# Performance work log

Measured on AMD Instinct MI355X. Metric: run time of the kernel, lower is better.

The kernel has to match this reference:

```python
import jax, jax.numpy as jnp
import numpy as np

B = 4096          # events
L = 524288        # total set points (avg 128 per event)
CIN = 16          # per-point feature size (set feature 'a')
DVEC = 32         # flat feature size (feature 'b')
PHI = [128, 128, 64]
MLP = [256, 128]
EPS = 1e-5        # BatchNorm1d eps


def setup_inputs() -> dict:
    key = jax.random.key(0)
    ks = jax.random.split(key, 10)
    def n(k, shape, scale=0.05):
        return jax.random.normal(k, shape, dtype=jnp.float32) * scale
    return {
        "x_a": jax.random.normal(ks[0], (1, CIN, L), dtype=jnp.float32),
        "x_b": jax.random.normal(ks[1], (B, DVEC), dtype=jnp.float32),
        # row 0 -> counts for set feature 'a'; row 1 ignored (Reshape branch)
        "sample_indices": jnp.full((2, B), L // B, dtype=jnp.int32),
        "W1": n(ks[2], (PHI[0], CIN)),  "b1": jnp.zeros((PHI[0],), jnp.float32),
        "W2": n(ks[3], (PHI[1], PHI[0])), "b2": jnp.zeros((PHI[1],), jnp.float32),
        "W3": n(ks[4], (PHI[2], PHI[1])), "b3": jnp.zeros((PHI[2],), jnp.float32),
        "Wm1": n(ks[5], (MLP[0], PHI[2] + DVEC)), "bm1": jnp.zeros((MLP[0],), jnp.float32),
        "g1": jnp.ones((MLP[0],), jnp.float32), "be1": jnp.zeros((MLP[0],), jnp.float32),
        "Wm2": n(ks[6], (MLP[1], MLP[0])), "bm2": jnp.zeros((MLP[1],), jnp.float32),
        "g2": jnp.ones((MLP[1],), jnp.float32), "be2": jnp.zeros((MLP[1],), jnp.float32),
        "Wm3": n(ks[7], (1, MLP[1])), "bm3": jnp.zeros((1,), jnp.float32),
    }


def _bn(x, g, b):
    # BatchNorm1d, training-mode batch stats, biased variance (torch semantics)
    mu = jnp.mean(x, axis=0)
    var = jnp.var(x, axis=0)
    return (x - mu) * jax.lax.rsqrt(var + EPS) * g + b


def reference(x_a, x_b, sample_indices,
              W1, b1, W2, b2, W3, b3,
              Wm1, bm1, g1, be1, Wm2, bm2, g2, be2, Wm3, bm3):
    counts = sample_indices[0].astype(jnp.int32)                       # [B]
    bounds = jnp.concatenate([jnp.zeros((1,), jnp.int32), jnp.cumsum(counts)])  # [B+1]

    # PhiNet: pointwise Conv1d stack (kernel size 1) on [CIN, L]
    h = x_a[0]
    h = jax.nn.relu(jnp.einsum('oc,cl->ol', W1, h) + b1[:, None])
    h = jax.nn.relu(jnp.einsum('oc,cl->ol', W2, h) + b2[:, None])
    h = jax.nn.relu(jnp.einsum('oc,cl->ol', W3, h) + b3[:, None])      # [64, L]

    # fused segment-mean: point p belongs to segment j iff bounds[j] <= p < bounds[j+1]
    seg = jnp.searchsorted(bounds, jnp.arange(h.shape[1], dtype=jnp.int32), side='right') - 1
    sums = jax.ops.segment_sum(h.T, seg, num_segments=counts.shape[0])  # [B, 64]
    means = sums / jnp.maximum(counts, 1).astype(jnp.float32)[:, None]

    # feature order: sorted keys -> ('a' set repr, 'b' flat)
    z = jnp.concatenate([means, x_b.reshape(-1, DVEC)], axis=1)        # [B, 96]

    z = jax.nn.relu(_bn(z @ Wm1.T + bm1, g1, be1))
    z = jax.nn.relu(_bn(z @ Wm2.T + bm2, g2, be2))
    return jax.nn.sigmoid(z @ Wm3.T + bm3)                             # [B, 1]
```

## Files before the change

kernel.cpp:

```cpp
#include <hip/hip_runtime.h>
#include <hip/hip_bf16.h>

#define B_EVENTS 4096
#define L_PTS    524288
#define CIN      16
#define C1       128
#define C2       128
#define C3       64
#define DVEC     32
#define ZDIM     96
#define M1       256
#define M2       128
#define BN_EPS   1e-5f
#define TPTS     64

typedef __attribute__((ext_vector_type(8))) short bf16x8;
typedef __attribute__((ext_vector_type(4))) float f32x4;

__device__ __forceinline__ ushort f2bf(float x) {
    union { float f; unsigned u; } a; a.f = x;
    unsigned r = (a.u + 0x7fffu + ((a.u >> 16) & 1u)) >> 16;
    return (ushort)r;
}

__device__ __forceinline__ int ldsoff(int base, int rowSlots, int c, int sir) {
    int s = c * rowSlots + sir;
    s ^= (c & 7);
    return base + s * 16;
}

__global__ __launch_bounds__(1024) void scan_zero_kernel(const int* __restrict__ si,
                                                         int* __restrict__ bounds,
                                                         float* __restrict__ stats) {
    __shared__ int sh[1024];
    const int tid = threadIdx.x;
    const int c0 = si[tid*4+0], c1 = si[tid*4+1], c2 = si[tid*4+2], c3 = si[tid*4+3];
    const int s4 = c0 + c1 + c2 + c3;
    sh[tid] = s4;
    if (tid < 768) stats[tid] = 0.f;
    __syncthreads();
    for (int off = 1; off < 1024; off <<= 1) {
        int add = (tid >= off) ? sh[tid - off] : 0;
        __syncthreads();
        sh[tid] += add;
        __syncthreads();
    }
    const int excl = (tid == 0) ? 0 : sh[tid - 1];
    bounds[tid*4+0] = excl;
    bounds[tid*4+1] = excl + c0;
    bounds[tid*4+2] = excl + c0 + c1;
    bounds[tid*4+3] = excl + c0 + c1 + c2;
    if (tid == 1023) bounds[B_EVENTS] = excl + s4;
}

__global__ __launch_bounds__(256) void prep_kernel(
    const float* __restrict__ W1, const float* __restrict__ W2, const float* __restrict__ W3,
    ushort* __restrict__ w1p, ushort* __restrict__ w2b, ushort* __restrict__ w3b)
{
    const int tid = blockIdx.x * 256 + threadIdx.x;
    const int nthr = gridDim.x * 256;
    for (int i = tid; i < C1 * 32; i += nthr) {
        const int r = i >> 5, k = i & 31;
        w1p[i] = (k < CIN) ? f2bf(W1[r * CIN + k]) : (ushort)0;
    }
    for (int i = tid; i < C2 * C1; i += nthr) w2b[i] = f2bf(W2[i]);
    for (int i = tid; i < C3 * C2; i += nthr) w3b[i] = f2bf(W3[i]);
}

__global__ __launch_bounds__(256, 2) void phi_mfma_kernel(
    const float* __restrict__ xa, const float* __restrict__ xb,
    const int* __restrict__ bounds,
    const ushort* __restrict__ w1p, const ushort* __restrict__ w2b, const ushort* __restrict__ w3b,
    const float* __restrict__ b1, const float* __restrict__ b2, const float* __restrict__ b3,
    float* __restrict__ z)
{
    __shared__ __align__(16) char lds[36864];
    __shared__ float msum[C3];

    const int tid  = threadIdx.x;
    const int lane = tid & 63;
    const int wid  = tid >> 6;
    const int wm   = wid >> 1;
    const int wn   = wid & 1;
    const int g4   = lane >> 4;
    const int c16  = lane & 15;

    bf16x8 a1[4], a2[4][4], a3[2][4];
    {
        const int r1 = wm * 64 + c16;
        #pragma unroll
        for (int mf = 0; mf < 4; ++mf)
            a1[mf] = *(const bf16x8*)&w1p[(r1 + mf * 16) * 32 + g4 * 8];
        #pragma unroll
        for (int mf = 0; mf < 4; ++mf)
            #pragma unroll
            for (int kf = 0; kf < 4; ++kf)
                a2[mf][kf] = *(const bf16x8*)&w2b[(r1 + mf * 16) * C1 + kf * 32 + g4 * 8];
        const int r3 = wm * 32 + c16;
        #pragma unroll
        for (int mf = 0; mf < 2; ++mf)
            #pragma unroll
            for (int kf = 0; kf < 4; ++kf)
                a3[mf][kf] = *(const bf16x8*)&w3b[(r3 + mf * 16) * C2 + kf * 32 + g4 * 8];
    }

    const int j     = blockIdx.x;
    const int start = bounds[j];
    const int cnt   = bounds[j + 1] - start;

    *(f32x4*)(lds + tid * 16) = f32x4{0.f, 0.f, 0.f, 0.f};
    if (tid < C3) msum[tid] = 0.f;

    const int pt   = tid & 63;
    const int half = tid >> 6;

    for (int p0 = 0; p0 < cnt; p0 += TPTS) {
        __syncthreads();

        {
            const int p = p0 + pt;
            union { ushort u[4]; unsigned long long ll; } pk;
            #pragma unroll
            for (int jj = 0; jj < 4; ++jj) {
                const float v = (p < cnt) ? xa[(size_t)(half * 4 + jj) * L_PTS + start + p] : 0.f;
                pk.u[jj] = f2bf(v);
            }
            *(unsigned long long*)(lds + ldsoff(0, 4, pt, half >> 1) + (half & 1) * 8) = pk.ll;
        }
        __syncthreads();

        {
            f32x4 acc[4][2];
            #pragma unroll
            for (int mf = 0; mf < 4; ++mf) {
                const f32x4 bb = *(const f32x4*)&b1[wm * 64 + mf * 16 + g4 * 4];
                acc[mf][0] = bb; acc[mf][1] = bb;
            }
            #pragma unroll
            for (int nf = 0; nf < 2; ++nf) {
                const int c = wn * 32 + nf * 16 + c16;
                const bf16x8 bfrag = *(const bf16x8*)(lds + ldsoff(0, 4, c, g4));
                #pragma unroll
                for (int mf = 0; mf < 4; ++mf)
                    acc[mf][nf] = __builtin_amdgcn_mfma_f32_16x16x32_bf16(a1[mf], bfrag, acc[mf][nf], 0, 0, 0);
            }
            #pragma unroll
            for (int mf = 0; mf < 4; ++mf)
                #pragma unroll
                for (int nf = 0; nf < 2; ++nf) {
                    const int c = wn * 32 + nf * 16 + c16;
                    union { ushort u[4]; unsigned long long ll; } pk;
                    #pragma unroll
                    for (int r = 0; r < 4; ++r) pk.u[r] = f2bf(fmaxf(acc[mf][nf][r], 0.f));
                    const int sir = (wm * 64 + mf * 16) / 8 + (g4 >> 1);
                    *(unsigned long long*)(lds + ldsoff(4096, 16, c, sir) + (g4 & 1) * 8) = pk.ll;
                }
        }
        __syncthreads();

        {
            f32x4 acc[4][2];
            #pragma unroll
            for (int mf = 0; mf < 4; ++mf) {
                const f32x4 bb = *(const f32x4*)&b2[wm * 64 + mf * 16 + g4 * 4];
                acc[mf][0] = bb; acc[mf][1] = bb;
            }
            #pragma unroll
            for (int nf = 0; nf < 2; ++nf) {
                const int c = wn * 32 + nf * 16 + c16;
                bf16x8 bk[4];
                #pragma unroll
                for (int kf = 0; kf < 4; ++kf)
                    bk[kf] = *(const bf16x8*)(lds + ldsoff(4096, 16, c, kf * 4 + g4));
                #pragma unroll
                for (int mf = 0; mf < 4; ++mf)
                    #pragma unroll
                    for (int kf = 0; kf < 4; ++kf)
                        acc[mf][nf] = __builtin_amdgcn_mfma_f32_16x16x32_bf16(a2[mf][kf], bk[kf], acc[mf][nf], 0, 0, 0);
            }
            #pragma unroll
            for (int mf = 0; mf < 4; ++mf)
                #pragma unroll
                for (int nf = 0; nf < 2; ++nf) {
                    const int c = wn * 32 + nf * 16 + c16;
                    union { ushort u[4]; unsigned long long ll; } pk;
                    #pragma unroll
                    for (int r = 0; r < 4; ++r) pk.u[r] = f2bf(fmaxf(acc[mf][nf][r], 0.f));
                    const int sir = (wm * 64 + mf * 16) / 8 + (g4 >> 1);
                    *(unsigned long long*)(lds + ldsoff(20480, 16, c, sir) + (g4 & 1) * 8) = pk.ll;
                }
        }
        __syncthreads();

        {
            f32x4 acc3[2][2];
            #pragma unroll
            for (int mf = 0; mf < 2; ++mf) {
                const f32x4 bb = *(const f32x4*)&b3[wm * 32 + mf * 16 + g4 * 4];
                acc3[mf][0] = bb; acc3[mf][1] = bb;
            }
            #pragma unroll
            for (int nf = 0; nf < 2; ++nf) {
                const int c = wn * 32 + nf * 16 + c16;
                bf16x8 bk[4];
                #pragma unroll
                for (int kf = 0; kf < 4; ++kf)
                    bk[kf] = *(const bf16x8*)(lds + ldsoff(20480, 16, c, kf * 4 + g4));
                #pragma unroll
                for (int mf = 0; mf < 2; ++mf)
                    #pragma unroll
                    for (int kf = 0; kf < 4; ++kf)
                        acc3[mf][nf] = __builtin_amdgcn_mfma_f32_16x16x32_bf16(a3[mf][kf], bk[kf], acc3[mf][nf], 0, 0, 0);
            }
            float s[2][4];
            #pragma unroll
            for (int mf = 0; mf < 2; ++mf)
                #pragma unroll
                for (int r = 0; r < 4; ++r) s[mf][r] = 0.f;
            #pragma unroll
            for (int nf = 0; nf < 2; ++nf) {
                const int col = p0 + wn * 32 + nf * 16 + c16;
                const bool valid = col < cnt;
                #pragma unroll
                for (int mf = 0; mf < 2; ++mf)
                    #pragma unroll
                    for (int r = 0; r < 4; ++r) {
                        const float v = fmaxf(acc3[mf][nf][r], 0.f);
                        if (valid) s[mf][r] += v;
                    }
            }
            #pragma unroll
            for (int mf = 0; mf < 2; ++mf)
                #pragma unroll
                for (int r = 0; r < 4; ++r) {
                    float v = s[mf][r];
                    #pragma unroll
                    for (int m = 1; m < 16; m <<= 1) v += __shfl_xor(v, m, 64);
                    s[mf][r] = v;
                }
            if (c16 == 0) {
                #pragma unroll
                for (int mf = 0; mf < 2; ++mf)
                    #pragma unroll
                    for (int r = 0; r < 4; ++r)
                        atomicAdd(&msum[wm * 32 + mf * 16 + g4 * 4 + r], s[mf][r]);
            }
        }
    }
    __syncthreads();

    if (tid < C3) {
        const float inv = 1.f / (float)max(cnt, 1);
        z[(size_t)j * ZDIM + tid] = msum[tid] * inv;
    } else if (tid < ZDIM) {
        z[(size_t)j * ZDIM + tid] = xb[(size_t)j * DVEC + (tid - C3)];
    }
}

__global__ __launch_bounds__(256) void mlp1_kernel(
    const float* __restrict__ z, const float* __restrict__ Wm1, const float* __restrict__ bm1,
    float* __restrict__ y1, float* __restrict__ gsum, float* __restrict__ gsq)
{
    __shared__ float zs[16][ZDIM + 4];
    const int r0 = blockIdx.x * 16;
    const int tid = threadIdx.x;
    for (int i = tid; i < 16 * ZDIM; i += 256) {
        const int r = i / ZDIM, c = i - r * ZDIM;
        zs[r][c] = z[(size_t)(r0 + r) * ZDIM + c];
    }
    __syncthreads();
    const int o = tid;
    float acc[16];
    const float bb = bm1[o];
    #pragma unroll
    for (int r = 0; r < 16; ++r) acc[r] = bb;
    for (int c = 0; c < ZDIM; c += 4) {
        const float4 w = *(const float4*)&Wm1[o * ZDIM + c];
        #pragma unroll
        for (int r = 0; r < 16; ++r) {
            const float4 v = *(const float4*)&zs[r][c];
            acc[r] += w.x*v.x + w.y*v.y + w.z*v.z + w.w*v.w;
        }
    }
    float s = 0.f, sq = 0.f;
    #pragma unroll
    for (int r = 0; r < 16; ++r) {
        y1[(size_t)(r0 + r) * M1 + o] = acc[r];
        s += acc[r]; sq += acc[r] * acc[r];
    }
    atomicAdd(&gsum[o], s);
    atomicAdd(&gsq[o], sq);
}

__global__ void bnfin_kernel(const float* __restrict__ gsum, const float* __restrict__ gsq,
                             const float* __restrict__ g, const float* __restrict__ be,
                             float* __restrict__ scale, float* __restrict__ shift, int n)
{
    const int o = blockIdx.x * blockDim.x + threadIdx.x;
    if (o >= n) return;
    const float mu  = gsum[o] * (1.f / B_EVENTS);
    const float var = gsq[o] * (1.f / B_EVENTS) - mu * mu;
    const float rs  = rsqrtf(var + BN_EPS);
    const float sc  = rs * g[o];
    scale[o] = sc;
    shift[o] = be[o] - mu * sc;
}

__global__ __launch_bounds__(256) void mlp2_kernel(
    const float* __restrict__ y1, const float* __restrict__ scale1, const float* __restrict__ shift1,
    const float* __restrict__ Wm2, const float* __restrict__ bm2,
    float* __restrict__ y2, float* __restrict__ gsum, float* __restrict__ gsq)
{
    __shared__ float zs[16][M1 + 4];
    const int r0 = blockIdx.x * 16;
    const int tid = threadIdx.x;
    for (int i = tid; i < 16 * M1; i += 256) {
        const int r = i >> 8, c = i & (M1 - 1);
        const float v = y1[(size_t)(r0 + r) * M1 + c];
        zs[r][c] = fmaxf(v * scale1[c] + shift1[c], 0.f);
    }
    __syncthreads();
    const int o = tid & 127;
    const int h = tid >> 7;
    float acc[8];
    const float bb = bm2[o];
    #pragma unroll
    for (int r = 0; r < 8; ++r) acc[r] = bb;
    for (int c = 0; c < M1; c += 4) {
        const float4 w = *(const float4*)&Wm2[o * M1 + c];
        #pragma unroll
        for (int r = 0; r < 8; ++r) {
            const float4 v = *(const float4*)&zs[h * 8 + r][c];
            acc[r] += w.x*v.x + w.y*v.y + w.z*v.z + w.w*v.w;
        }
    }
    float s = 0.f, sq = 0.f;
    #pragma unroll
    for (int r = 0; r < 8; ++r) {
        y2[(size_t)(r0 + h * 8 + r) * M2 + o] = acc[r];
        s += acc[r]; sq += acc[r] * acc[r];
    }
    atomicAdd(&gsum[o], s);
    atomicAdd(&gsq[o], sq);
}

__global__ __launch_bounds__(256) void final_kernel(
    const float* __restrict__ y2, const float* __restrict__ scale2, const float* __restrict__ shift2,
    const float* __restrict__ Wm3, const float* __restrict__ bm3,
    float* __restrict__ out)
{
    const int tid = threadIdx.x;
    const int w = tid >> 6, l = tid & 63;
    const int r = blockIdx.x * 4 + w;
    const float e0 = fmaxf(y2[(size_t)r * M2 + l]      * scale2[l]      + shift2[l],      0.f);
    const float e1 = fmaxf(y2[(size_t)r * M2 + 64 + l] * scale2[64 + l] + shift2[64 + l], 0.f);
    float a = e0 * Wm3[l] + e1 * Wm3[64 + l];
    #pragma unroll
    for (int off = 32; off >= 1; off >>= 1) a += __shfl_down(a, off, 64);
    if (l == 0) out[r] = 1.f / (1.f + expf(-(a + bm3[0])));
}

extern "C" void kernel_launch(void* const* d_in, const int* in_sizes, int n_in,
                              void* d_out, int out_size, void* d_ws, size_t ws_size,
                              hipStream_t stream) {
    const float* xa  = (const float*)d_in[0];
    const float* xb  = (const float*)d_in[1];
    const int*   si  = (const int*)  d_in[2];
    const float* W1  = (const float*)d_in[3];
    const float* b1  = (const float*)d_in[4];
    const float* W2  = (const float*)d_in[5];
    const float* b2  = (const float*)d_in[6];
    const float* W3  = (const float*)d_in[7];
    const float* b3  = (const float*)d_in[8];
    const float* Wm1 = (const float*)d_in[9];
    const float* bm1 = (const float*)d_in[10];
    const float* g1  = (const float*)d_in[11];
    const float* be1 = (const float*)d_in[12];
    const float* Wm2 = (const float*)d_in[13];
    const float* bm2 = (const float*)d_in[14];
    const float* g2  = (const float*)d_in[15];
    const float* be2 = (const float*)d_in[16];
    const float* Wm3 = (const float*)d_in[17];
    const float* bm3 = (const float*)d_in[18];
    float* out = (float*)d_out;

    char* ws = (char*)d_ws;
    size_t off = 0;
    auto alloc = [&](size_t bytes) -> void* {
        void* p = ws + off;
        off = (off + bytes + 255) & ~(size_t)255;
        return p;
    };
    int*    bounds = (int*)   alloc((B_EVENTS + 1) * sizeof(int));
    float*  stats  = (float*) alloc(768 * sizeof(float));
    float*  z      = (float*) alloc((size_t)B_EVENTS * ZDIM * sizeof(float));
    float*  y1     = (float*) alloc((size_t)B_EVENTS * M1 * sizeof(float));
    float*  y2     = (float*) alloc((size_t)B_EVENTS * M2 * sizeof(float));
    float*  scale1 = (float*) alloc(M1 * sizeof(float));
    float*  shift1 = (float*) alloc(M1 * sizeof(float));
    float*  scale2 = (float*) alloc(M2 * sizeof(float));
    float*  shift2 = (float*) alloc(M2 * sizeof(float));
    ushort* w1p    = (ushort*)alloc(C1 * 32 * sizeof(ushort));
    ushort* w2b    = (ushort*)alloc(C2 * C1 * sizeof(ushort));
    ushort* w3b    = (ushort*)alloc(C3 * C2 * sizeof(ushort));
    float* gsum1 = stats;
    float* gsq1  = stats + 256;
    float* gsum2 = stats + 512;
    float* gsq2  = stats + 640;

    hipLaunchKernelGGL(scan_zero_kernel, dim3(1), dim3(1024), 0, stream, si, bounds, stats);
    hipLaunchKernelGGL(prep_kernel, dim3(16), dim3(256), 0, stream, W1, W2, W3, w1p, w2b, w3b);
    hipLaunchKernelGGL(phi_mfma_kernel, dim3(B_EVENTS), dim3(256), 0, stream,
                       xa, xb, bounds, w1p, w2b, w3b, b1, b2, b3, z);
    hipLaunchKernelGGL(mlp1_kernel, dim3(B_EVENTS / 16), dim3(256), 0, stream,
                       z, Wm1, bm1, y1, gsum1, gsq1);
    hipLaunchKernelGGL(bnfin_kernel, dim3(1), dim3(256), 0, stream,
                       gsum1, gsq1, g1, be1, scale1, shift1, M1);
    hipLaunchKernelGGL(mlp2_kernel, dim3(B_EVENTS / 16), dim3(256), 0, stream,
                       y1, scale1, shift1, Wm2, bm2, y2, gsum2, gsq2);
    hipLaunchKernelGGL(bnfin_kernel, dim3(1), dim3(128), 0, stream,
                       gsum2, gsq2, g2, be2, scale2, shift2, M2);
    hipLaunchKernelGGL(final_kernel, dim3(B_EVENTS / 4), dim3(256), 0, stream,
                       y2, scale2, shift2, Wm3, bm3, out);
}
```

Baseline: 150.1 us.

## Process several events per block with prefetched point loads and packed bf16 converts

```diff
diff --git a/kernel.cpp b/kernel.cpp
--- a/kernel.cpp
+++ b/kernel.cpp
@@ -13,6 +13,7 @@
 #define M2       128
 #define BN_EPS   1e-5f
 #define TPTS     64
+#define EPB      4
 
 typedef __attribute__((ext_vector_type(8))) short bf16x8;
 typedef __attribute__((ext_vector_type(4))) float f32x4;
@@ -21,6 +22,19 @@
     union { float f; unsigned u; } a; a.f = x;
     unsigned r = (a.u + 0x7fffu + ((a.u >> 16) & 1u)) >> 16;
     return (ushort)r;
+}
+
+__device__ __forceinline__ unsigned cvtpk(float lo, float hi) {
+    unsigned r;
+    asm("v_cvt_pk_bf16_f32 %0, %1, %2" : "=v"(r) : "v"(lo), "v"(hi));
+    return r;
+}
+
+__device__ __forceinline__ unsigned long long pack4relu(f32x4 a) {
+    union { unsigned u[2]; unsigned long long ll; } pk;
+    pk.u[0] = cvtpk(fmaxf(a[0], 0.f), fmaxf(a[1], 0.f));
+    pk.u[1] = cvtpk(fmaxf(a[2], 0.f), fmaxf(a[3], 0.f));
+    return pk.ll;
 }
 
 __device__ __forceinline__ int ldsoff(int base, int rowSlots, int c, int sir) {
@@ -104,156 +118,173 @@
                 a3[mf][kf] = *(const bf16x8*)&w3b[(r3 + mf * 16) * C2 + kf * 32 + g4 * 8];
     }
 
-    const int j     = blockIdx.x;
-    const int start = bounds[j];
-    const int cnt   = bounds[j + 1] - start;
-
-    *(f32x4*)(lds + tid * 16) = f32x4{0.f, 0.f, 0.f, 0.f};
-    if (tid < C3) msum[tid] = 0.f;
-
     const int pt   = tid & 63;
     const int half = tid >> 6;
-
-    for (int p0 = 0; p0 < cnt; p0 += TPTS) {
-        __syncthreads();
-
+    const int xoff = ldsoff(0, 4, pt, half >> 1) + (half & 1) * 8;
+
+    for (int e = 0; e < EPB; ++e) {
+        const int j     = blockIdx.x * EPB + e;
+        const int start = bounds[j];
+        const int cnt   = bounds[j + 1] - start;
+
+        if (tid < C3) msum[tid] = 0.f;
+
+        float xr[4];
+        #pragma unroll
+        for (int jj = 0; jj < 4; ++jj)
+            xr[jj] = (pt < cnt) ? xa[(size_t)(half * 4 + jj) * L_PTS + start + pt] : 0.f;
         {
-            const int p = p0 + pt;
-            union { ushort u[4]; unsigned long long ll; } pk;
-            #pragma unroll
-            for (int jj = 0; jj < 4; ++jj) {
-                const float v = (p < cnt) ? xa[(size_t)(half * 4 + jj) * L_PTS + start + p] : 0.f;
-                pk.u[jj] = f2bf(v);
-            }
-            *(unsigned long long*)(lds + ldsoff(0, 4, pt, half >> 1) + (half & 1) * 8) = pk.ll;
+            union { unsigned u[2]; unsigned long long ll; } pk;
+            pk.u[0] = cvtpk(xr[0], xr[1]);
+            pk.u[1] = cvtpk(xr[2], xr[3]);
+            *(unsigned long long*)(lds + xoff) = pk.ll;
         }
         __syncthreads();
 
-        {
-            f32x4 acc[4][2];
-            #pragma unroll
-            for (int mf = 0; mf < 4; ++mf) {
-                const f32x4 bb = *(const f32x4*)&b1[wm * 64 + mf * 16 + g4 * 4];
-                acc[mf][0] = bb; acc[mf][1] = bb;
+        for (int p0 = 0; p0 < cnt; p0 += TPTS) {
+            const bool more = (p0 + TPTS) < cnt;
+
+            if (more) {
+                const int p = p0 + TPTS + pt;
+                #pragma unroll
+                for (int jj = 0; jj < 4; ++jj)
+                    xr[jj] = (p < cnt) ? xa[(size_t)(half * 4 + jj) * L_PTS + start + p] : 0.f;
             }
-            #pragma unroll
-            for (int nf = 0; nf < 2; ++nf) {
-                const int c = wn * 32 + nf * 16 + c16;
-                const bf16x8 bfrag = *(const bf16x8*)(lds + ldsoff(0, 4, c, g4));
+
+            {
+                f32x4 acc[4][2];
+                #pragma unroll
+                for (int mf = 0; mf < 4; ++mf) {
+                    const f32x4 bb = *(const f32x4*)&b1[wm * 64 + mf * 16 + g4 * 4];
+                    acc[mf][0] = bb; acc[mf][1] = bb;
+                }
+                bf16x8 bfrag[2];
+                #pragma unroll
+                for (int nf = 0; nf < 2; ++nf)
+                    bfrag[nf] = *(const bf16x8*)(lds + ldsoff(0, 4, wn * 32 + nf * 16 + c16, g4));
+                __builtin_amdgcn_s_setprio(1);
+                #pragma unroll
+                for (int nf = 0; nf < 2; ++nf)
+                    #pragma unroll
+                    for (int mf = 0; mf < 4; ++mf)
+                        acc[mf][nf] = __builtin_amdgcn_mfma_f32_16x16x32_bf16(a1[mf], bfrag[nf], acc[mf][nf], 0, 0, 0);
+                __builtin_amdgcn_s_setprio(0);
                 #pragma unroll
                 for (int mf = 0; mf < 4; ++mf)
-                    acc[mf][nf] = __builtin_amdgcn_mfma_f32_16x16x32_bf16(a1[mf], bfrag, acc[mf][nf], 0, 0, 0);
+                    #pragma unroll
+                    for (int nf = 0; nf < 2; ++nf) {
+                        const int c = wn * 32 + nf * 16 + c16;
+                        const int sir = (wm * 64 + mf * 16) / 8 + (g4 >> 1);
+                        *(unsigned long long*)(lds + ldsoff(4096, 16, c, sir) + (g4 & 1) * 8) = pack4relu(acc[mf][nf]);
+                    }
             }
-            #pragma unroll
-            for (int mf = 0; mf < 4; ++mf)
+            __syncthreads();
+
+            {
+                f32x4 acc[4][2];
+                #pragma unroll
+                for (int mf = 0; mf < 4; ++mf) {
+                    const f32x4 bb = *(const f32x4*)&b2[wm * 64 + mf * 16 + g4 * 4];
+                    acc[mf][0] = bb; acc[mf][1] = bb;
+                }
                 #pragma unroll
                 for (int nf = 0; nf < 2; ++nf) {
                     const int c = wn * 32 + nf * 16 + c16;
-                    union { ushort u[4]; unsigned long long ll; } pk;
-                    #pragma unroll
-                    for (int r = 0; r < 4; ++r) pk.u[r] = f2bf(fmaxf(acc[mf][nf][r], 0.f));
-                    const int sir = (wm * 64 + mf * 16) / 8 + (g4 >> 1);
-                    *(unsigned long long*)(lds + ldsoff(4096, 16, c, sir) + (g4 & 1) * 8) = pk.ll;
-                }
-        }
-        __syncthreads();
-
-        {
-            f32x4 acc[4][2];
-            #pragma unroll
-            for (int mf = 0; mf < 4; ++mf) {
-                const f32x4 bb = *(const f32x4*)&b2[wm * 64 + mf * 16 + g4 * 4];
-                acc[mf][0] = bb; acc[mf][1] = bb;
+                    bf16x8 bk[4];
+                    #pragma unroll
+                    for (int kf = 0; kf < 4; ++kf)
+                        bk[kf] = *(const bf16x8*)(lds + ldsoff(4096, 16, c, kf * 4 + g4));
+                    __builtin_amdgcn_s_setprio(1);
+                    #pragma unroll
+                    for (int mf = 0; mf < 4; ++mf)
+                        #pragma unroll
+                        for (int kf = 0; kf < 4; ++kf)
+                            acc[mf][nf] = __builtin_amdgcn_mfma_f32_16x16x32_bf16(a2[mf][kf], bk[kf], acc[mf][nf], 0, 0, 0);
+                    __builtin_amdgcn_s_setprio(0);
+                }
+                #pragma unroll
+                for (int mf = 0; mf < 4; ++mf)
+                    #pragma unroll
+                    for (int nf = 0; nf < 2; ++nf) {
+                        const int c = wn * 32 + nf * 16 + c16;
+                        const int sir = (wm * 64 + mf * 16) / 8 + (g4 >> 1);
+                        *(unsigned long long*)(lds + ldsoff(20480, 16, c, sir) + (g4 & 1) * 8) = pack4relu(acc[mf][nf]);
+                    }
             }
-            #pragma unroll
-            for (int nf = 0; nf < 2; ++nf) {
-                const int c = wn * 32 + nf * 16 + c16;
-                bf16x8 bk[4];
-                #pragma unroll
-                for (int kf = 0; kf < 4; ++kf)
-                    bk[kf] = *(const bf16x8*)(lds + ldsoff(4096, 16, c, kf * 4 + g4));
-                #pragma unroll
-                for (int mf = 0; mf < 4; ++mf)
-                    #pragma unroll
-                    for (int kf = 0; kf < 4; ++kf)
-                        acc[mf][nf] = __builtin_amdgcn_mfma_f32_16x16x32_bf16(a2[mf][kf], bk[kf], acc[mf][nf], 0, 0, 0);
+            __syncthreads();
+
+            if (more) {
+                union { unsigned u[2]; unsigned long long ll; } pk;
+                pk.u[0] = cvtpk(xr[0], xr[1]);
+                pk.u[1] = cvtpk(xr[2], xr[3]);
+                *(unsigned long long*)(lds + xoff) = pk.ll;
             }
-            #pragma unroll
-            for (int mf = 0; mf < 4; ++mf)
+
+            {
+                f32x4 acc3[2][2];
+                #pragma unroll
+                for (int mf = 0; mf < 2; ++mf) {
+                    const f32x4 bb = *(const f32x4*)&b3[wm * 32 + mf * 16 + g4 * 4];
+                    acc3[mf][0] = bb; acc3[mf][1] = bb;
+                }
                 #pragma unroll
                 for (int nf = 0; nf < 2; ++nf) {
                     const int c = wn * 32 + nf * 16 + c16;
-                    union { ushort u[4]; unsigned long long ll; } pk;
-                    #pragma unroll
-                    for (int r = 0; r < 4; ++r) pk.u[r] = f2bf(fmaxf(acc[mf][nf][r], 0.f));
-                    const int sir = (wm * 64 + mf * 16) / 8 + (g4 >> 1);
-                    *(unsigned long long*)(lds + ldsoff(20480, 16, c, sir) + (g4 & 1) * 8) = pk.ll;
-                }
+                    bf16x8 bk[4];
+                    #pragma unroll
+                    for (int kf = 0; kf < 4; ++kf)
+                        bk[kf] = *(const bf16x8*)(lds + ldsoff(20480, 16, c, kf * 4 + g4));
+                    __builtin_amdgcn_s_setprio(1);
+                    #pragma unroll
+                    for (int mf = 0; mf < 2; ++mf)
+                        #pragma unroll
+                        for (int kf = 0; kf < 4; ++kf)
+                            acc3[mf][nf] = __builtin_amdgcn_mfma_f32_16x16x32_bf16(a3[mf][kf], bk[kf], acc3[mf][nf], 0, 0, 0);
+                    __builtin_amdgcn_s_setprio(0);
+                }
+                float s[2][4];
+                #pragma unroll
+                for (int mf = 0; mf < 2; ++mf)
+                    #pragma unroll
+                    for (int r = 0; r < 4; ++r) s[mf][r] = 0.f;
+                #pragma unroll
+                for (int nf = 0; nf < 2; ++nf) {
+                    const int col = p0 + wn * 32 + nf * 16 + c16;
+                    const bool valid = col < cnt;
+                    #pragma unroll
+                    for (int mf = 0; mf < 2; ++mf)
+                        #pragma unroll
+                        for (int r = 0; r < 4; ++r) {
+                            const float v = fmaxf(acc3[mf][nf][r], 0.f);
+                            if (valid) s[mf][r] += v;
+                        }
+                }
+                #pragma unroll
+                for (int mf = 0; mf < 2; ++mf)
+                    #pragma unroll
+                    for (int r = 0; r < 4; ++r) {
+                        float v = s[mf][r];
+                        #pragma unroll
+                        for (int m = 1; m < 16; m <<= 1) v += __shfl_xor(v, m, 64);
+                        s[mf][r] = v;
+                    }
+                if (c16 == 0) {
+                    #pragma unroll
+                    for (int mf = 0; mf < 2; ++mf)
+                        #pragma unroll
+                        for (int r = 0; r < 4; ++r)
+                            atomicAdd(&msum[wm * 32 + mf * 16 + g4 * 4 + r], s[mf][r]);
+                }
+            }
+            __syncthreads();
         }
-        __syncthreads();
-
-        {
-            f32x4 acc3[2][2];
-            #pragma unroll
-            for (int mf = 0; mf < 2; ++mf) {
-                const f32x4 bb = *(const f32x4*)&b3[wm * 32 + mf * 16 + g4 * 4];
-                acc3[mf][0] = bb; acc3[mf][1] = bb;
-            }
-            #pragma unroll
-            for (int nf = 0; nf < 2; ++nf) {
-                const int c = wn * 32 + nf * 16 + c16;
-                bf16x8 bk[4];
-                #pragma unroll
-                for (int kf = 0; kf < 4; ++kf)
-                    bk[kf] = *(const bf16x8*)(lds + ldsoff(20480, 16, c, kf * 4 + g4));
-                #pragma unroll
-                for (int mf = 0; mf < 2; ++mf)
-                    #pragma unroll
-                    for (int kf = 0; kf < 4; ++kf)
-                        acc3[mf][nf] = __builtin_amdgcn_mfma_f32_16x16x32_bf16(a3[mf][kf], bk[kf], acc3[mf][nf], 0, 0, 0);
-            }
-            float s[2][4];
-            #pragma unroll
-            for (int mf = 0; mf < 2; ++mf)
-                #pragma unroll
-                for (int r = 0; r < 4; ++r) s[mf][r] = 0.f;
-            #pragma unroll
-            for (int nf = 0; nf < 2; ++nf) {
-                const int col = p0 + wn * 32 + nf * 16 + c16;
-                const bool valid = col < cnt;
-                #pragma unroll
-                for (int mf = 0; mf < 2; ++mf)
-                    #pragma unroll
-                    for (int r = 0; r < 4; ++r) {
-                        const float v = fmaxf(acc3[mf][nf][r], 0.f);
-                        if (valid) s[mf][r] += v;
-                    }
-            }
-            #pragma unroll
-            for (int mf = 0; mf < 2; ++mf)
-                #pragma unroll
-                for (int r = 0; r < 4; ++r) {
-                    float v = s[mf][r];
-                    #pragma unroll
-                    for (int m = 1; m < 16; m <<= 1) v += __shfl_xor(v, m, 64);
-                    s[mf][r] = v;
-                }
-            if (c16 == 0) {
-                #pragma unroll
-                for (int mf = 0; mf < 2; ++mf)
-                    #pragma unroll
-                    for (int r = 0; r < 4; ++r)
-                        atomicAdd(&msum[wm * 32 + mf * 16 + g4 * 4 + r], s[mf][r]);
-            }
+
+        if (tid < C3) {
+            const float inv = 1.f / (float)max(cnt, 1);
+            z[(size_t)j * ZDIM + tid] = msum[tid] * inv;
+        } else if (tid < ZDIM) {
+            z[(size_t)j * ZDIM + tid] = xb[(size_t)j * DVEC + (tid - C3)];
         }
-    }
-    __syncthreads();
-
-    if (tid < C3) {
-        const float inv = 1.f / (float)max(cnt, 1);
-        z[(size_t)j * ZDIM + tid] = msum[tid] * inv;
-    } else if (tid < ZDIM) {
-        z[(size_t)j * ZDIM + tid] = xb[(size_t)j * DVEC + (tid - C3)];
     }
 }
 
@@ -410,7 +441,7 @@
 
     hipLaunchKernelGGL(scan_zero_kernel, dim3(1), dim3(1024), 0, stream, si, bounds, stats);
     hipLaunchKernelGGL(prep_kernel, dim3(16), dim3(256), 0, stream, W1, W2, W3, w1p, w2b, w3b);
-    hipLaunchKernelGGL(phi_mfma_kernel, dim3(B_EVENTS), dim3(256), 0, stream,
+    hipLaunchKernelGGL(phi_mfma_kernel, dim3(B_EVENTS / EPB), dim3(256), 0, stream,
                        xa, xb, bounds, w1p, w2b, w3b, b1, b2, b3, z);
     hipLaunchKernelGGL(mlp1_kernel, dim3(B_EVENTS / 16), dim3(256), 0, stream,
                        z, Wm1, bm1, y1, gsum1, gsq1);
```

Result: faster. 132.8 us (-11.5%).
